# Kernel tuning notes

Hardware: AMD Instinct MI355X
Metric: run time of the kernel (lower is better)

## Reference

```python
import jax, jax.numpy as jnp
import numpy as np


def setup_inputs() -> dict:
    key = jax.random.key(0)
    ks = jax.random.split(key, 6)
    B, L, D, H, U = 256, 225, 1280, 256, 256
    features = jax.random.normal(ks[0], (B, L, D), dtype=jnp.float32)
    hidden = jax.random.normal(ks[1], (B, H), dtype=jnp.float32)
    W1 = jax.random.normal(ks[2], (D, U), dtype=jnp.float32) * (1.0 / np.sqrt(D))
    b1 = jnp.zeros((U,), dtype=jnp.float32)
    W2 = jax.random.normal(ks[3], (H, U), dtype=jnp.float32) * (1.0 / np.sqrt(H))
    b2 = jnp.zeros((U,), dtype=jnp.float32)
    V = jax.random.normal(ks[4], (U, 1), dtype=jnp.float32) * (1.0 / np.sqrt(U))
    bV = jnp.zeros((1,), dtype=jnp.float32)
    return {"features": features, "hidden": hidden, "W1": W1, "b1": b1,
            "W2": W2, "b2": b2, "V": V, "bV": bV}


def reference(features, hidden, W1, b1, W2, b2, V, bV):
    # features: [B, L, D]; hidden: [B, H]
    proj_f = jnp.einsum('bld,du->blu', features, W1) + b1        # [B, L, U]
    proj_h = (hidden @ W2 + b2)[:, None, :]                      # [B, 1, U]
    score = jnp.tanh(proj_f + proj_h)                            # [B, L, U]
    logits = jnp.einsum('blu,uo->blo', score, V) + bV            # [B, L, 1]
    attn = jax.nn.softmax(logits, axis=1)                        # [B, L, 1]
    context = jnp.sum(attn * features, axis=1)                   # [B, D]
    return context
```

## Files before the change

kernel.cpp:

```cpp
#include <hip/hip_runtime.h>
#include <hip/hip_bf16.h>

#define B_ 256
#define L_ 225
#define D_ 1280
#define H_ 256
#define U_ 256

typedef __bf16  bf16x8 __attribute__((ext_vector_type(8)));
typedef float   f32x4  __attribute__((ext_vector_type(4)));
typedef unsigned short u16x8 __attribute__((ext_vector_type(8)));

__device__ __forceinline__ unsigned short f2bf(float f) {
    union { __hip_bfloat16 h; unsigned short u; } cv;
    cv.h = __float2bfloat16(f);
    return cv.u;
}

__device__ __forceinline__ void gload_lds16(const void* g, void* l) {
    __builtin_amdgcn_global_load_lds(
        (const __attribute__((address_space(1))) unsigned int*)g,
        (__attribute__((address_space(3))) unsigned int*)l,
        16, 0, 0);
}

__device__ __forceinline__ float wredmax(float x) {
#pragma unroll
    for (int off = 32; off > 0; off >>= 1) x = fmaxf(x, __shfl_xor(x, off, 64));
    return x;
}
__device__ __forceinline__ float wredsum(float x) {
#pragma unroll
    for (int off = 32; off > 0; off >>= 1) x += __shfl_xor(x, off, 64);
    return x;
}

__global__ void k_prep_w1t(const float* __restrict__ W1, __hip_bfloat16* __restrict__ w1t) {
    int idx = blockIdx.x * 256 + threadIdx.x;
    int k = idx / U_;
    int u = idx % U_;
    w1t[(size_t)u * D_ + k] = __float2bfloat16(W1[idx]);
}

__global__ void k_proj_h(const float* __restrict__ hidden, const float* __restrict__ W2,
                         const float* __restrict__ b1, const float* __restrict__ b2,
                         float* __restrict__ ph) {
    __shared__ float sh[H_];
    int b = blockIdx.x;
    int u = threadIdx.x;
    sh[u] = hidden[b * H_ + u];
    __syncthreads();
    float acc = b1[u] + b2[u];
#pragma unroll 8
    for (int h = 0; h < H_; ++h) acc += sh[h] * W2[h * U_ + u];
    ph[b * U_ + u] = acc;
}

__global__ __launch_bounds__(1024, 4) void k_fused(
        const float* __restrict__ feat,
        const __hip_bfloat16* __restrict__ w1t,
        const float* __restrict__ ph,
        const float* __restrict__ Vv,
        float* __restrict__ out) {
    __shared__ __align__(128) char smem[139392];
    float* sV   = (float*)(smem + 131072);
    float* sPh  = (float*)(smem + 132096);
    float* sL   = (float*)(smem + 133120);
    float* sLog = (float*)(smem + 137216);
    float* sAtt = (float*)(smem + 138240);
    float* sRed = (float*)(smem + 139264);
    float* sRed2= (float*)(smem + 139328);

    const int tid  = threadIdx.x;
    const int lane = tid & 63;
    const int wave = tid >> 6;
    const int wr   = wave >> 2;
    const int wc   = wave & 3;
    const int b    = blockIdx.x;

    if (tid < 256) { sV[tid] = Vv[tid]; sPh[tid] = ph[b * 256 + tid]; }

    const int ar    = tid >> 2;
    const int arc   = ar < L_ ? ar : (L_ - 1);
    const int akseg = (tid & 3) << 4;
    const float* aSrc0 = feat + ((size_t)(b * L_ + arc) * D_ + akseg);
    const int ac80  = akseg >> 3;
    char* const aDst0 = smem;

    f32x4 acc[4][4];
#pragma unroll
    for (int mi = 0; mi < 4; ++mi)
#pragma unroll
        for (int ni = 0; ni < 4; ++ni)
            acc[mi][ni] = (f32x4){0.f, 0.f, 0.f, 0.f};

    auto stage = [&](int kt, char* bufA, char* bufB) {
        const float* src = aSrc0 + kt * 64;
        f32x4 v0 = *reinterpret_cast<const f32x4*>(src);
        f32x4 v1 = *reinterpret_cast<const f32x4*>(src + 4);
        f32x4 v2 = *reinterpret_cast<const f32x4*>(src + 8);
        f32x4 v3 = *reinterpret_cast<const f32x4*>(src + 12);
#pragma unroll
        for (int pass = 0; pass < 2; ++pass) {
            int s   = pass * 1024 + tid;
            int u   = s >> 3;
            int c8s = s & 7;
            int c8g = c8s ^ (u & 7);
            gload_lds16(w1t + (size_t)u * D_ + kt * 64 + c8g * 8, bufB + s * 16);
        }
        u16x8 w0, w1;
        w0[0] = f2bf(v0[0]); w0[1] = f2bf(v0[1]); w0[2] = f2bf(v0[2]); w0[3] = f2bf(v0[3]);
        w0[4] = f2bf(v1[0]); w0[5] = f2bf(v1[1]); w0[6] = f2bf(v1[2]); w0[7] = f2bf(v1[3]);
        w1[0] = f2bf(v2[0]); w1[1] = f2bf(v2[1]); w1[2] = f2bf(v2[2]); w1[3] = f2bf(v2[3]);
        w1[4] = f2bf(v3[0]); w1[5] = f2bf(v3[1]); w1[6] = f2bf(v3[2]); w1[7] = f2bf(v3[3]);
        int swz = (ar & 7) << 4;
        *reinterpret_cast<u16x8*>(bufA + (ar << 7) + ((ac80 << 4) ^ swz))       = w0;
        *reinterpret_cast<u16x8*>(bufA + (ar << 7) + (((ac80 + 1) << 4) ^ swz)) = w1;
    };

    auto compute = [&](const char* bufA, const char* bufB) {
#pragma unroll
        for (int ks = 0; ks < 2; ++ks) {
            const int kk2 = (ks * 32 + ((lane >> 4) << 3)) * 2;
            bf16x8 a[4], bb[4];
#pragma unroll
            for (int mi = 0; mi < 4; ++mi) {
                int r = wr * 64 + mi * 16 + (lane & 15);
                a[mi] = *reinterpret_cast<const bf16x8*>(bufA + (r << 7) + (kk2 ^ ((r & 7) << 4)));
            }
#pragma unroll
            for (int ni = 0; ni < 4; ++ni) {
                int u = wc * 64 + ni * 16 + (lane & 15);
                bb[ni] = *reinterpret_cast<const bf16x8*>(bufB + (u << 7) + (kk2 ^ ((u & 7) << 4)));
            }
#pragma unroll
            for (int mi = 0; mi < 4; ++mi)
#pragma unroll
                for (int ni = 0; ni < 4; ++ni)
                    acc[mi][ni] = __builtin_amdgcn_mfma_f32_16x16x32_bf16(
                        a[mi], bb[ni], acc[mi][ni], 0, 0, 0);
        }
    };

    stage(0, smem, smem + 32768);
    __syncthreads();
    int cur = 0;
    for (int kt = 0; kt < 20; ++kt) {
        char* An = smem + (cur ^ 1) * 65536;
        if (kt < 19) stage(kt + 1, An, An + 32768);
        char* Ac = smem + cur * 65536;
        compute(Ac, Ac + 32768);
        __syncthreads();
        cur ^= 1;
    }

    float phu[4], vu[4];
#pragma unroll
    for (int ni = 0; ni < 4; ++ni) {
        int u = wc * 64 + ni * 16 + (lane & 15);
        phu[ni] = sPh[u];
        vu[ni]  = sV[u];
    }
#pragma unroll
    for (int mi = 0; mi < 4; ++mi) {
#pragma unroll
        for (int rg = 0; rg < 4; ++rg) {
            int row = wr * 64 + mi * 16 + ((lane >> 4) << 2) + rg;
            float s = 0.f;
#pragma unroll
            for (int ni = 0; ni < 4; ++ni) {
                float x = acc[mi][ni][rg] + phu[ni];
                float t = 1.f - 2.f / (__expf(2.f * x) + 1.f);
                s += t * vu[ni];
            }
            s += __shfl_xor(s, 1, 64);
            s += __shfl_xor(s, 2, 64);
            s += __shfl_xor(s, 4, 64);
            s += __shfl_xor(s, 8, 64);
            if ((lane & 15) == 0) sL[wc * 256 + row] = s;
        }
    }
    __syncthreads();
    if (tid < 256) sLog[tid] = sL[tid] + sL[256 + tid] + sL[512 + tid] + sL[768 + tid];
    __syncthreads();

    float x  = (tid < L_) ? sLog[tid] : -3.4e38f;
    float mx = wredmax(x);
    if (lane == 0) sRed[wave] = mx;
    __syncthreads();
    mx = sRed[0];
#pragma unroll
    for (int i = 1; i < 16; ++i) mx = fmaxf(mx, sRed[i]);
    float e  = (tid < L_) ? __expf(x - mx) : 0.f;
    float sm = wredsum(e);
    if (lane == 0) sRed2[wave] = sm;
    __syncthreads();
    sm = 0.f;
#pragma unroll
    for (int i = 0; i < 16; ++i) sm += sRed2[i];
    if (tid < L_) sAtt[tid] = e / sm;
    __syncthreads();

    f32x4 c[5];
#pragma unroll
    for (int ch = 0; ch < 5; ++ch) c[ch] = (f32x4){0.f, 0.f, 0.f, 0.f};
    for (int l = wave; l < L_; l += 16) {
        float a = sAtt[l];
        const float* fr = feat + (size_t)(b * L_ + l) * D_ + (lane << 2);
#pragma unroll
        for (int ch = 0; ch < 5; ++ch)
            c[ch] += a * *reinterpret_cast<const f32x4*>(fr + ch * 256);
    }
    float* pc = (float*)smem;
#pragma unroll
    for (int ch = 0; ch < 5; ++ch)
        *reinterpret_cast<f32x4*>(pc + wave * 1280 + ch * 256 + (lane << 2)) = c[ch];
    __syncthreads();
    if (tid < 320) {
        f32x4 s = (f32x4){0.f, 0.f, 0.f, 0.f};
#pragma unroll
        for (int w = 0; w < 16; ++w)
            s += *reinterpret_cast<const f32x4*>(pc + w * 1280 + (tid << 2));
        *reinterpret_cast<f32x4*>(out + (size_t)b * D_ + (tid << 2)) = s;
    }
}

extern "C" void kernel_launch(void* const* d_in, const int* in_sizes, int n_in,
                              void* d_out, int out_size, void* d_ws, size_t ws_size,
                              hipStream_t stream) {
    const float* feat   = (const float*)d_in[0];
    const float* hidden = (const float*)d_in[1];
    const float* W1     = (const float*)d_in[2];
    const float* b1     = (const float*)d_in[3];
    const float* W2     = (const float*)d_in[4];
    const float* b2     = (const float*)d_in[5];
    const float* Vv     = (const float*)d_in[6];

    char* ws = (char*)d_ws;
    __hip_bfloat16* w1t = (__hip_bfloat16*)(ws);
    float* ph = (float*)(ws + 655360);
    float* out = (float*)d_out;

    k_prep_w1t<<<(U_ * D_) / 256, 256, 0, stream>>>(W1, w1t);
    k_proj_h  <<<B_, U_, 0, stream>>>(hidden, W2, b1, b2, ph);
    k_fused   <<<B_, 1024, 0, stream>>>(feat, w1t, ph, Vv, out);
}
```

Before: 139.1 us.

## Tile sequence into 32-row chunks with online softmax, reusing LDS features

The sequence is processed in 32-row tiles. Each tile's full-K features are converted to bf16 and held in LDS, the W1 slices are streamed through double buffers, and an online-softmax running max and sum update the context accumulators from the same LDS copy. This removes the second global pass over the large feature tensor. In exchange, W1 is re-streamed once per tile, each tile hits many block-wide barriers, and the context is accumulated from bf16 rather than fp32 features, which may matter for accuracy. The leftover row 224 goes through a separate scalar path.

```diff
diff --git a/kernel.cpp b/kernel.cpp
--- a/kernel.cpp
+++ b/kernel.cpp
@@ -6,15 +6,25 @@
 #define D_ 1280
 #define H_ 256
 #define U_ 256
+#define LT 32
+#define NFT 7
 
 typedef __bf16  bf16x8 __attribute__((ext_vector_type(8)));
 typedef float   f32x4  __attribute__((ext_vector_type(4)));
 typedef unsigned short u16x8 __attribute__((ext_vector_type(8)));
+typedef unsigned short u16x4 __attribute__((ext_vector_type(4)));
 
 __device__ __forceinline__ unsigned short f2bf(float f) {
     union { __hip_bfloat16 h; unsigned short u; } cv;
     cv.h = __float2bfloat16(f);
     return cv.u;
+}
+
+__device__ __forceinline__ f32x4 bf4_to_f32(u16x4 w) {
+    union { unsigned u; float f; } a0, a1, a2, a3;
+    a0.u = (unsigned)w[0] << 16; a1.u = (unsigned)w[1] << 16;
+    a2.u = (unsigned)w[2] << 16; a3.u = (unsigned)w[3] << 16;
+    return (f32x4){a0.f, a1.f, a2.f, a3.f};
 }
 
 __device__ __forceinline__ void gload_lds16(const void* g, void* l) {
@@ -56,161 +66,195 @@
     ph[b * U_ + u] = acc;
 }
 
+__device__ __forceinline__ void stageB(const __hip_bfloat16* __restrict__ w1t,
+                                       char* buf, int kt, int tid) {
+#pragma unroll
+    for (int pass = 0; pass < 2; ++pass) {
+        int s   = pass * 1024 + tid;
+        int u   = s >> 3;
+        int c8s = s & 7;
+        int c8g = c8s ^ (u & 7);
+        gload_lds16(w1t + (size_t)u * D_ + kt * 64 + c8g * 8, buf + s * 16);
+    }
+}
+
 __global__ __launch_bounds__(1024, 4) void k_fused(
         const float* __restrict__ feat,
         const __hip_bfloat16* __restrict__ w1t,
         const float* __restrict__ ph,
         const float* __restrict__ Vv,
         float* __restrict__ out) {
-    __shared__ __align__(128) char smem[139392];
-    float* sV   = (float*)(smem + 131072);
-    float* sPh  = (float*)(smem + 132096);
-    float* sL   = (float*)(smem + 133120);
-    float* sLog = (float*)(smem + 137216);
-    float* sAtt = (float*)(smem + 138240);
-    float* sRed = (float*)(smem + 139264);
-    float* sRed2= (float*)(smem + 139328);
+    __shared__ __align__(128) char smem[150784];
+    char*  sB  = smem + 81920;
+    float* sV  = (float*)(smem + 147456);
+    float* sPh = (float*)(smem + 148480);
+    float* sLp = (float*)(smem + 149504);
+    float* sW  = (float*)(smem + 150528);
+    float* sSc = (float*)(smem + 150656);
 
     const int tid  = threadIdx.x;
     const int lane = tid & 63;
     const int wave = tid >> 6;
-    const int wr   = wave >> 2;
-    const int wc   = wave & 3;
+    const int wr   = wave >> 3;
+    const int wc   = wave & 7;
     const int b    = blockIdx.x;
 
     if (tid < 256) { sV[tid] = Vv[tid]; sPh[tid] = ph[b * 256 + tid]; }
 
-    const int ar    = tid >> 2;
-    const int arc   = ar < L_ ? ar : (L_ - 1);
-    const int akseg = (tid & 3) << 4;
-    const float* aSrc0 = feat + ((size_t)(b * L_ + arc) * D_ + akseg);
-    const int ac80  = akseg >> 3;
-    char* const aDst0 = smem;
-
-    f32x4 acc[4][4];
-#pragma unroll
-    for (int mi = 0; mi < 4; ++mi)
-#pragma unroll
-        for (int ni = 0; ni < 4; ++ni)
-            acc[mi][ni] = (f32x4){0.f, 0.f, 0.f, 0.f};
-
-    auto stage = [&](int kt, char* bufA, char* bufB) {
-        const float* src = aSrc0 + kt * 64;
-        f32x4 v0 = *reinterpret_cast<const f32x4*>(src);
-        f32x4 v1 = *reinterpret_cast<const f32x4*>(src + 4);
-        f32x4 v2 = *reinterpret_cast<const f32x4*>(src + 8);
-        f32x4 v3 = *reinterpret_cast<const f32x4*>(src + 12);
-#pragma unroll
-        for (int pass = 0; pass < 2; ++pass) {
-            int s   = pass * 1024 + tid;
-            int u   = s >> 3;
-            int c8s = s & 7;
-            int c8g = c8s ^ (u & 7);
-            gload_lds16(w1t + (size_t)u * D_ + kt * 64 + c8g * 8, bufB + s * 16);
-        }
-        u16x8 w0, w1;
-        w0[0] = f2bf(v0[0]); w0[1] = f2bf(v0[1]); w0[2] = f2bf(v0[2]); w0[3] = f2bf(v0[3]);
-        w0[4] = f2bf(v1[0]); w0[5] = f2bf(v1[1]); w0[6] = f2bf(v1[2]); w0[7] = f2bf(v1[3]);
-        w1[0] = f2bf(v2[0]); w1[1] = f2bf(v2[1]); w1[2] = f2bf(v2[2]); w1[3] = f2bf(v2[3]);
-        w1[4] = f2bf(v3[0]); w1[5] = f2bf(v3[1]); w1[6] = f2bf(v3[2]); w1[7] = f2bf(v3[3]);
-        int swz = (ar & 7) << 4;
-        *reinterpret_cast<u16x8*>(bufA + (ar << 7) + ((ac80 << 4) ^ swz))       = w0;
-        *reinterpret_cast<u16x8*>(bufA + (ar << 7) + (((ac80 + 1) << 4) ^ swz)) = w1;
-    };
-
-    auto compute = [&](const char* bufA, const char* bufB) {
-#pragma unroll
-        for (int ks = 0; ks < 2; ++ks) {
-            const int kk2 = (ks * 32 + ((lane >> 4) << 3)) * 2;
-            bf16x8 a[4], bb[4];
-#pragma unroll
-            for (int mi = 0; mi < 4; ++mi) {
-                int r = wr * 64 + mi * 16 + (lane & 15);
-                a[mi] = *reinterpret_cast<const bf16x8*>(bufA + (r << 7) + (kk2 ^ ((r & 7) << 4)));
+    const float* featB = feat + (size_t)b * L_ * D_;
+
+    f32x4 c[5];
+#pragma unroll
+    for (int ch = 0; ch < 5; ++ch) c[ch] = (f32x4){0.f, 0.f, 0.f, 0.f};
+    float m_run = -3.0e38f, s_run = 0.f;
+
+    for (int t = 0; t < NFT; ++t) {
+        __syncthreads();
+
+#pragma unroll
+        for (int p = 0; p < 10; ++p) {
+            int idx = tid + p * 1024;
+            int r   = idx / 320;
+            int c4  = idx - r * 320;
+            f32x4 v = *reinterpret_cast<const f32x4*>(
+                featB + (size_t)(t * LT + r) * D_ + c4 * 4);
+            u16x4 w;
+            w[0] = f2bf(v[0]); w[1] = f2bf(v[1]); w[2] = f2bf(v[2]); w[3] = f2bf(v[3]);
+            *reinterpret_cast<u16x4*>(smem + r * 2560 + ((c4 * 8) ^ ((r & 7) << 4))) = w;
+        }
+        stageB(w1t, sB, 0, tid);
+        __syncthreads();
+
+        f32x4 acc0 = (f32x4){0.f, 0.f, 0.f, 0.f};
+        f32x4 acc1 = (f32x4){0.f, 0.f, 0.f, 0.f};
+        int cur = 0;
+        const int r  = wr * 16 + (lane & 15);
+        const int u0 = wc * 32 + (lane & 15);
+        const int aswz = (r & 7) << 4;
+        const int bswz = (u0 & 7) << 4;
+        for (int kt = 0; kt < 20; ++kt) {
+            if (kt < 19) stageB(w1t, sB + (cur ^ 1) * 32768, kt + 1, tid);
+            const char* bufB = sB + cur * 32768;
+#pragma unroll
+            for (int ks = 0; ks < 2; ++ks) {
+                int kloc = ks * 64 + ((lane >> 4) << 4);
+                bf16x8 a = *reinterpret_cast<const bf16x8*>(
+                    smem + r * 2560 + ((kt * 128 + kloc) ^ aswz));
+                bf16x8 b0 = *reinterpret_cast<const bf16x8*>(
+                    bufB + u0 * 128 + (kloc ^ bswz));
+                bf16x8 b1 = *reinterpret_cast<const bf16x8*>(
+                    bufB + (u0 + 16) * 128 + (kloc ^ bswz));
+                acc0 = __builtin_amdgcn_mfma_f32_16x16x32_bf16(a, b0, acc0, 0, 0, 0);
+                acc1 = __builtin_amdgcn_mfma_f32_16x16x32_bf16(a, b1, acc1, 0, 0, 0);
             }
-#pragma unroll
-            for (int ni = 0; ni < 4; ++ni) {
-                int u = wc * 64 + ni * 16 + (lane & 15);
-                bb[ni] = *reinterpret_cast<const bf16x8*>(bufB + (u << 7) + (kk2 ^ ((u & 7) << 4)));
+            __syncthreads();
+            cur ^= 1;
+        }
+
+        float ph0 = sPh[u0], ph1 = sPh[u0 + 16];
+        float v0  = sV[u0],  v1  = sV[u0 + 16];
+#pragma unroll
+        for (int rg = 0; rg < 4; ++rg) {
+            int row = wr * 16 + ((lane >> 4) << 2) + rg;
+            float x0 = acc0[rg] + ph0;
+            float x1 = acc1[rg] + ph1;
+            float sl = (1.f - 2.f / (__expf(2.f * x0) + 1.f)) * v0
+                     + (1.f - 2.f / (__expf(2.f * x1) + 1.f)) * v1;
+            sl += __shfl_xor(sl, 1, 64);
+            sl += __shfl_xor(sl, 2, 64);
+            sl += __shfl_xor(sl, 4, 64);
+            sl += __shfl_xor(sl, 8, 64);
+            if ((lane & 15) == 0) sLp[wc * 32 + row] = sl;
+        }
+        __syncthreads();
+
+        if (wave == 0) {
+            float lg = -3.0e38f;
+            if (lane < 32) {
+                lg = 0.f;
+#pragma unroll
+                for (int w8 = 0; w8 < 8; ++w8) lg += sLp[w8 * 32 + lane];
             }
-#pragma unroll
-            for (int mi = 0; mi < 4; ++mi)
-#pragma unroll
-                for (int ni = 0; ni < 4; ++ni)
-                    acc[mi][ni] = __builtin_amdgcn_mfma_f32_16x16x32_bf16(
-                        a[mi], bb[ni], acc[mi][ni], 0, 0, 0);
-        }
-    };
-
-    stage(0, smem, smem + 32768);
-    __syncthreads();
-    int cur = 0;
-    for (int kt = 0; kt < 20; ++kt) {
-        char* An = smem + (cur ^ 1) * 65536;
-        if (kt < 19) stage(kt + 1, An, An + 32768);
-        char* Ac = smem + cur * 65536;
-        compute(Ac, Ac + 32768);
-        __syncthreads();
-        cur ^= 1;
-    }
-
-    float phu[4], vu[4];
-#pragma unroll
-    for (int ni = 0; ni < 4; ++ni) {
-        int u = wc * 64 + ni * 16 + (lane & 15);
-        phu[ni] = sPh[u];
-        vu[ni]  = sV[u];
-    }
-#pragma unroll
-    for (int mi = 0; mi < 4; ++mi) {
-#pragma unroll
-        for (int rg = 0; rg < 4; ++rg) {
-            int row = wr * 64 + mi * 16 + ((lane >> 4) << 2) + rg;
-            float s = 0.f;
-#pragma unroll
-            for (int ni = 0; ni < 4; ++ni) {
-                float x = acc[mi][ni][rg] + phu[ni];
-                float t = 1.f - 2.f / (__expf(2.f * x) + 1.f);
-                s += t * vu[ni];
+            float tmax = wredmax(lg);
+            float nm   = fmaxf(m_run, tmax);
+            float wv   = (lane < 32) ? __expf(lg - nm) : 0.f;
+            float ts   = wredsum(wv);
+            float rs   = __expf(m_run - nm);
+            s_run = s_run * rs + ts;
+            m_run = nm;
+            if (lane < 32) sW[lane] = wv;
+            if (lane == 0) sSc[0] = rs;
+        }
+        __syncthreads();
+
+        float rs = sSc[0];
+#pragma unroll
+        for (int ch = 0; ch < 5; ++ch) c[ch] *= rs;
+#pragma unroll
+        for (int rp = 0; rp < 2; ++rp) {
+            int rr = wave + rp * 16;
+            float wgt = sW[rr];
+            const char* arow = smem + rr * 2560;
+            int rswz = (rr & 7) << 4;
+#pragma unroll
+            for (int ch = 0; ch < 5; ++ch) {
+                u16x4 w4 = *reinterpret_cast<const u16x4*>(
+                    arow + ((ch * 512 + lane * 8) ^ rswz));
+                c[ch] += wgt * bf4_to_f32(w4);
             }
-            s += __shfl_xor(s, 1, 64);
-            s += __shfl_xor(s, 2, 64);
-            s += __shfl_xor(s, 4, 64);
-            s += __shfl_xor(s, 8, 64);
-            if ((lane & 15) == 0) sL[wc * 256 + row] = s;
-        }
-    }
-    __syncthreads();
-    if (tid < 256) sLog[tid] = sL[tid] + sL[256 + tid] + sL[512 + tid] + sL[768 + tid];
-    __syncthreads();
-
-    float x  = (tid < L_) ? sLog[tid] : -3.4e38f;
-    float mx = wredmax(x);
-    if (lane == 0) sRed[wave] = mx;
-    __syncthreads();
-    mx = sRed[0];
-#pragma unroll
-    for (int i = 1; i < 16; ++i) mx = fmaxf(mx, sRed[i]);
-    float e  = (tid < L_) ? __expf(x - mx) : 0.f;
-    float sm = wredsum(e);
-    if (lane == 0) sRed2[wave] = sm;
-    __syncthreads();
-    sm = 0.f;
-#pragma unroll
-    for (int i = 0; i < 16; ++i) sm += sRed2[i];
-    if (tid < L_) sAtt[tid] = e / sm;
-    __syncthreads();
-
-    f32x4 c[5];
-#pragma unroll
-    for (int ch = 0; ch < 5; ++ch) c[ch] = (f32x4){0.f, 0.f, 0.f, 0.f};
-    for (int l = wave; l < L_; l += 16) {
-        float a = sAtt[l];
-        const float* fr = feat + (size_t)(b * L_ + l) * D_ + (lane << 2);
-#pragma unroll
-        for (int ch = 0; ch < 5; ++ch)
-            c[ch] += a * *reinterpret_cast<const f32x4*>(fr + ch * 256);
-    }
+        }
+    }
+
+    {
+        const float* frow = featB + (size_t)224 * D_;
+        int u  = wave * 16 + (lane & 15);
+        int kq = lane >> 4;
+        const float* fk = frow + kq * 320;
+        const __hip_bfloat16* wk = w1t + (size_t)u * D_ + kq * 320;
+        float dot = 0.f;
+#pragma unroll 8
+        for (int i = 0; i < 80; ++i) {
+            f32x4 fv = *reinterpret_cast<const f32x4*>(fk + i * 4);
+            u16x4 w4 = *reinterpret_cast<const u16x4*>(wk + i * 4);
+            f32x4 wf = bf4_to_f32(w4);
+            dot += fv[0] * wf[0] + fv[1] * wf[1] + fv[2] * wf[2] + fv[3] * wf[3];
+        }
+        dot += __shfl_xor(dot, 16, 64);
+        dot += __shfl_xor(dot, 32, 64);
+        float xg = dot + sPh[u];
+        float sv = (1.f - 2.f / (__expf(2.f * xg) + 1.f)) * sV[u];
+        sv += __shfl_xor(sv, 1, 64);
+        sv += __shfl_xor(sv, 2, 64);
+        sv += __shfl_xor(sv, 4, 64);
+        sv += __shfl_xor(sv, 8, 64);
+        if (lane == 0) sLp[wave] = sv;
+    }
+    __syncthreads();
+    if (wave == 0) {
+        float lg = 0.f;
+#pragma unroll
+        for (int i = 0; i < 16; ++i) lg += sLp[i];
+        float nm = fmaxf(m_run, lg);
+        float wv = __expf(lg - nm);
+        float rs = __expf(m_run - nm);
+        s_run = s_run * rs + wv;
+        if (lane == 0) { sSc[0] = rs; sSc[1] = s_run; sW[0] = wv; }
+    }
+    __syncthreads();
+    {
+        float rs = sSc[0];
+#pragma unroll
+        for (int ch = 0; ch < 5; ++ch) c[ch] *= rs;
+        if (wave == 0) {
+            float wgt = sW[0];
+            const float* frow = featB + (size_t)224 * D_;
+#pragma unroll
+            for (int ch = 0; ch < 5; ++ch)
+                c[ch] += wgt * *reinterpret_cast<const f32x4*>(frow + ch * 256 + lane * 4);
+        }
+    }
+
+    __syncthreads();
     float* pc = (float*)smem;
 #pragma unroll
     for (int ch = 0; ch < 5; ++ch)
@@ -221,6 +265,8 @@
 #pragma unroll
         for (int w = 0; w < 16; ++w)
             s += *reinterpret_cast<const f32x4*>(pc + w * 1280 + (tid << 2));
+        float inv = 1.f / sSc[1];
+        s *= inv;
         *reinterpret_cast<f32x4*>(out + (size_t)b * D_ + (tid << 2)) = s;
     }
 }
```

Result: slower. 336.8 us (+142.2%).

## Spill bf16 features to workspace for context pass; drop softmax max-subtraction

Applied to the files above, without the earlier changes.

During the GEMM staging, each block writes its bf16-converted feature tile to a workspace buffer. The context-sum pass then rereads that half-size bf16 copy instead of the fp32 features, which roughly halves the second read, at the cost of an extra global write of the same size. The softmax skips the max reduction and normalizes once at the end, which removes several barriers but risks overflow for large logits. The A-tile LDS store is moved after the MFMA compute to overlap global loads, and the context loop is unrolled by two rows.

```diff
diff --git a/kernel.cpp b/kernel.cpp
--- a/kernel.cpp
+++ b/kernel.cpp
@@ -10,11 +10,19 @@
 typedef __bf16  bf16x8 __attribute__((ext_vector_type(8)));
 typedef float   f32x4  __attribute__((ext_vector_type(4)));
 typedef unsigned short u16x8 __attribute__((ext_vector_type(8)));
+typedef unsigned short u16x4 __attribute__((ext_vector_type(4)));
 
 __device__ __forceinline__ unsigned short f2bf(float f) {
     union { __hip_bfloat16 h; unsigned short u; } cv;
     cv.h = __float2bfloat16(f);
     return cv.u;
+}
+
+__device__ __forceinline__ f32x4 bf4_to_f32(u16x4 w) {
+    union { unsigned u; float f; } a0, a1, a2, a3;
+    a0.u = (unsigned)w[0] << 16; a1.u = (unsigned)w[1] << 16;
+    a2.u = (unsigned)w[2] << 16; a3.u = (unsigned)w[3] << 16;
+    return (f32x4){a0.f, a1.f, a2.f, a3.f};
 }
 
 __device__ __forceinline__ void gload_lds16(const void* g, void* l) {
@@ -24,11 +32,6 @@
         16, 0, 0);
 }
 
-__device__ __forceinline__ float wredmax(float x) {
-#pragma unroll
-    for (int off = 32; off > 0; off >>= 1) x = fmaxf(x, __shfl_xor(x, off, 64));
-    return x;
-}
 __device__ __forceinline__ float wredsum(float x) {
 #pragma unroll
     for (int off = 32; off > 0; off >>= 1) x += __shfl_xor(x, off, 64);
@@ -56,20 +59,22 @@
     ph[b * U_ + u] = acc;
 }
 
-__global__ __launch_bounds__(1024, 4) void k_fused(
+__global__ __launch_bounds__(1024) void __attribute__((noinline)) k_dummy() {}
+
+template<int BF16WS>
+__global__ __launch_bounds__(1024) void k_fused(
         const float* __restrict__ feat,
         const __hip_bfloat16* __restrict__ w1t,
         const float* __restrict__ ph,
         const float* __restrict__ Vv,
+        __hip_bfloat16* __restrict__ fbf,
         float* __restrict__ out) {
-    __shared__ __align__(128) char smem[139392];
+    __shared__ __align__(128) char smem[138304];
     float* sV   = (float*)(smem + 131072);
     float* sPh  = (float*)(smem + 132096);
     float* sL   = (float*)(smem + 133120);
-    float* sLog = (float*)(smem + 137216);
-    float* sAtt = (float*)(smem + 138240);
-    float* sRed = (float*)(smem + 139264);
-    float* sRed2= (float*)(smem + 139328);
+    float* sW   = (float*)(smem + 137216);
+    float* sRed = (float*)(smem + 138240);
 
     const int tid  = threadIdx.x;
     const int lane = tid & 63;
@@ -84,8 +89,9 @@
     const int arc   = ar < L_ ? ar : (L_ - 1);
     const int akseg = (tid & 3) << 4;
     const float* aSrc0 = feat + ((size_t)(b * L_ + arc) * D_ + akseg);
-    const int ac80  = akseg >> 3;
-    char* const aDst0 = smem;
+    __hip_bfloat16* fDst0 = fbf + ((size_t)(b * L_ + arc) * D_ + akseg);
+    const int ac80 = akseg >> 3;
+    const int aswz = (ar & 7) << 4;
 
     f32x4 acc[4][4];
 #pragma unroll
@@ -94,12 +100,14 @@
         for (int ni = 0; ni < 4; ++ni)
             acc[mi][ni] = (f32x4){0.f, 0.f, 0.f, 0.f};
 
-    auto stage = [&](int kt, char* bufA, char* bufB) {
+    auto loadA = [&](int kt, f32x4* v) {
         const float* src = aSrc0 + kt * 64;
-        f32x4 v0 = *reinterpret_cast<const f32x4*>(src);
-        f32x4 v1 = *reinterpret_cast<const f32x4*>(src + 4);
-        f32x4 v2 = *reinterpret_cast<const f32x4*>(src + 8);
-        f32x4 v3 = *reinterpret_cast<const f32x4*>(src + 12);
+        v[0] = *reinterpret_cast<const f32x4*>(src);
+        v[1] = *reinterpret_cast<const f32x4*>(src + 4);
+        v[2] = *reinterpret_cast<const f32x4*>(src + 8);
+        v[3] = *reinterpret_cast<const f32x4*>(src + 12);
+    };
+    auto stageB = [&](int kt, char* bufB) {
 #pragma unroll
         for (int pass = 0; pass < 2; ++pass) {
             int s   = pass * 1024 + tid;
@@ -108,16 +116,20 @@
             int c8g = c8s ^ (u & 7);
             gload_lds16(w1t + (size_t)u * D_ + kt * 64 + c8g * 8, bufB + s * 16);
         }
+    };
+    auto storeA = [&](int kt, const f32x4* v, char* bufA) {
         u16x8 w0, w1;
-        w0[0] = f2bf(v0[0]); w0[1] = f2bf(v0[1]); w0[2] = f2bf(v0[2]); w0[3] = f2bf(v0[3]);
-        w0[4] = f2bf(v1[0]); w0[5] = f2bf(v1[1]); w0[6] = f2bf(v1[2]); w0[7] = f2bf(v1[3]);
-        w1[0] = f2bf(v2[0]); w1[1] = f2bf(v2[1]); w1[2] = f2bf(v2[2]); w1[3] = f2bf(v2[3]);
-        w1[4] = f2bf(v3[0]); w1[5] = f2bf(v3[1]); w1[6] = f2bf(v3[2]); w1[7] = f2bf(v3[3]);
-        int swz = (ar & 7) << 4;
-        *reinterpret_cast<u16x8*>(bufA + (ar << 7) + ((ac80 << 4) ^ swz))       = w0;
-        *reinterpret_cast<u16x8*>(bufA + (ar << 7) + (((ac80 + 1) << 4) ^ swz)) = w1;
+        w0[0] = f2bf(v[0][0]); w0[1] = f2bf(v[0][1]); w0[2] = f2bf(v[0][2]); w0[3] = f2bf(v[0][3]);
+        w0[4] = f2bf(v[1][0]); w0[5] = f2bf(v[1][1]); w0[6] = f2bf(v[1][2]); w0[7] = f2bf(v[1][3]);
+        w1[0] = f2bf(v[2][0]); w1[1] = f2bf(v[2][1]); w1[2] = f2bf(v[2][2]); w1[3] = f2bf(v[2][3]);
+        w1[4] = f2bf(v[3][0]); w1[5] = f2bf(v[3][1]); w1[6] = f2bf(v[3][2]); w1[7] = f2bf(v[3][3]);
+        *reinterpret_cast<u16x8*>(bufA + (ar << 7) + ((ac80 << 4) ^ aswz))       = w0;
+        *reinterpret_cast<u16x8*>(bufA + (ar << 7) + (((ac80 + 1) << 4) ^ aswz)) = w1;
+        if (BF16WS && ar < L_) {
+            *reinterpret_cast<u16x8*>(fDst0 + kt * 64)     = w0;
+            *reinterpret_cast<u16x8*>(fDst0 + kt * 64 + 8) = w1;
+        }
     };
-
     auto compute = [&](const char* bufA, const char* bufB) {
 #pragma unroll
         for (int ks = 0; ks < 2; ++ks) {
@@ -142,14 +154,21 @@
         }
     };
 
-    stage(0, smem, smem + 32768);
+    {
+        f32x4 v[4];
+        loadA(0, v);
+        stageB(0, smem + 32768);
+        storeA(0, v, smem);
+    }
     __syncthreads();
     int cur = 0;
     for (int kt = 0; kt < 20; ++kt) {
-        char* An = smem + (cur ^ 1) * 65536;
-        if (kt < 19) stage(kt + 1, An, An + 32768);
-        char* Ac = smem + cur * 65536;
-        compute(Ac, Ac + 32768);
+        char* bufN = smem + (cur ^ 1) * 65536;
+        f32x4 v[4];
+        if (kt < 19) { loadA(kt + 1, v); stageB(kt + 1, bufN + 32768); }
+        char* bufC = smem + cur * 65536;
+        compute(bufC, bufC + 32768);
+        if (kt < 19) storeA(kt + 1, v, bufN);
         __syncthreads();
         cur ^= 1;
     }
@@ -170,8 +189,7 @@
 #pragma unroll
             for (int ni = 0; ni < 4; ++ni) {
                 float x = acc[mi][ni][rg] + phu[ni];
-                float t = 1.f - 2.f / (__expf(2.f * x) + 1.f);
-                s += t * vu[ni];
+                s += (1.f - 2.f / (__expf(2.f * x) + 1.f)) * vu[ni];
             }
             s += __shfl_xor(s, 1, 64);
             s += __shfl_xor(s, 2, 64);
@@ -181,46 +199,100 @@
         }
     }
     __syncthreads();
-    if (tid < 256) sLog[tid] = sL[tid] + sL[256 + tid] + sL[512 + tid] + sL[768 + tid];
-    __syncthreads();
-
-    float x  = (tid < L_) ? sLog[tid] : -3.4e38f;
-    float mx = wredmax(x);
-    if (lane == 0) sRed[wave] = mx;
-    __syncthreads();
-    mx = sRed[0];
-#pragma unroll
-    for (int i = 1; i < 16; ++i) mx = fmaxf(mx, sRed[i]);
-    float e  = (tid < L_) ? __expf(x - mx) : 0.f;
-    float sm = wredsum(e);
-    if (lane == 0) sRed2[wave] = sm;
-    __syncthreads();
-    sm = 0.f;
-#pragma unroll
-    for (int i = 0; i < 16; ++i) sm += sRed2[i];
-    if (tid < L_) sAtt[tid] = e / sm;
+    float den_p = 0.f;
+    if (tid < 256) {
+        float lg = sL[tid] + sL[256 + tid] + sL[512 + tid] + sL[768 + tid];
+        float w  = (tid < L_) ? __expf(lg) : 0.f;
+        sW[tid] = w;
+        den_p = w;
+    }
+    den_p = wredsum(den_p);
+    if (lane == 0) sRed[wave] = den_p;
     __syncthreads();
 
     f32x4 c[5];
 #pragma unroll
     for (int ch = 0; ch < 5; ++ch) c[ch] = (f32x4){0.f, 0.f, 0.f, 0.f};
-    for (int l = wave; l < L_; l += 16) {
-        float a = sAtt[l];
-        const float* fr = feat + (size_t)(b * L_ + l) * D_ + (lane << 2);
+
+    if (BF16WS) {
+        const char* fB = (const char*)(fbf + (size_t)b * L_ * D_);
+        int l = wave;
+        for (; l + 16 < L_; l += 32) {
+            float wa = sW[l], wb = sW[l + 16];
+            const char* ra = fB + (size_t)l * 2560;
+            const char* rb = fB + (size_t)(l + 16) * 2560;
+            u16x8 a0 = *reinterpret_cast<const u16x8*>(ra + lane * 16);
+            u16x8 a1 = *reinterpret_cast<const u16x8*>(ra + 1024 + lane * 16);
+            u16x4 a2 = *reinterpret_cast<const u16x4*>(ra + 2048 + lane * 8);
+            u16x8 b0 = *reinterpret_cast<const u16x8*>(rb + lane * 16);
+            u16x8 b1 = *reinterpret_cast<const u16x8*>(rb + 1024 + lane * 16);
+            u16x4 b2 = *reinterpret_cast<const u16x4*>(rb + 2048 + lane * 8);
+            c[0] += wa * bf4_to_f32((u16x4){a0[0],a0[1],a0[2],a0[3]});
+            c[1] += wa * bf4_to_f32((u16x4){a0[4],a0[5],a0[6],a0[7]});
+            c[2] += wa * bf4_to_f32((u16x4){a1[0],a1[1],a1[2],a1[3]});
+            c[3] += wa * bf4_to_f32((u16x4){a1[4],a1[5],a1[6],a1[7]});
+            c[4] += wa * bf4_to_f32(a2);
+            c[0] += wb * bf4_to_f32((u16x4){b0[0],b0[1],b0[2],b0[3]});
+            c[1] += wb * bf4_to_f32((u16x4){b0[4],b0[5],b0[6],b0[7]});
+            c[2] += wb * bf4_to_f32((u16x4){b1[0],b1[1],b1[2],b1[3]});
+            c[3] += wb * bf4_to_f32((u16x4){b1[4],b1[5],b1[6],b1[7]});
+            c[4] += wb * bf4_to_f32(b2);
+        }
+        if (l < L_) {
+            float wa = sW[l];
+            const char* ra = fB + (size_t)l * 2560;
+            u16x8 a0 = *reinterpret_cast<const u16x8*>(ra + lane * 16);
+            u16x8 a1 = *reinterpret_cast<const u16x8*>(ra + 1024 + lane * 16);
+            u16x4 a2 = *reinterpret_cast<const u16x4*>(ra + 2048 + lane * 8);
+            c[0] += wa * bf4_to_f32((u16x4){a0[0],a0[1],a0[2],a0[3]});
+            c[1] += wa * bf4_to_f32((u16x4){a0[4],a0[5],a0[6],a0[7]});
+            c[2] += wa * bf4_to_f32((u16x4){a1[0],a1[1],a1[2],a1[3]});
+            c[3] += wa * bf4_to_f32((u16x4){a1[4],a1[5],a1[6],a1[7]});
+            c[4] += wa * bf4_to_f32(a2);
+        }
+    } else {
+        const float* fB = feat + (size_t)b * L_ * D_;
+        int l = wave;
+        for (; l + 16 < L_; l += 32) {
+            float wa = sW[l], wb = sW[l + 16];
+            const float* ra = fB + (size_t)l * D_ + (lane << 2);
+            const float* rb = fB + (size_t)(l + 16) * D_ + (lane << 2);
+#pragma unroll
+            for (int ch = 0; ch < 5; ++ch) {
+                c[ch] += wa * *reinterpret_cast<const f32x4*>(ra + ch * 256);
+                c[ch] += wb * *reinterpret_cast<const f32x4*>(rb + ch * 256);
+            }
+        }
+        if (l < L_) {
+            float wa = sW[l];
+            const float* ra = fB + (size_t)l * D_ + (lane << 2);
+#pragma unroll
+            for (int ch = 0; ch < 5; ++ch)
+                c[ch] += wa * *reinterpret_cast<const f32x4*>(ra + ch * 256);
+        }
+    }
+
+    float* pc = (float*)smem;
+    if (BF16WS) {
+#pragma unroll
+        for (int ch = 0; ch < 4; ++ch)
+            *reinterpret_cast<f32x4*>(pc + wave * 1280 + (ch >> 1) * 512 + lane * 8 + (ch & 1) * 4) = c[ch];
+        *reinterpret_cast<f32x4*>(pc + wave * 1280 + 1024 + lane * 4) = c[4];
+    } else {
 #pragma unroll
         for (int ch = 0; ch < 5; ++ch)
-            c[ch] += a * *reinterpret_cast<const f32x4*>(fr + ch * 256);
-    }
-    float* pc = (float*)smem;
-#pragma unroll
-    for (int ch = 0; ch < 5; ++ch)
-        *reinterpret_cast<f32x4*>(pc + wave * 1280 + ch * 256 + (lane << 2)) = c[ch];
+            *reinterpret_cast<f32x4*>(pc + wave * 1280 + ch * 256 + (lane << 2)) = c[ch];
+    }
     __syncthreads();
     if (tid < 320) {
         f32x4 s = (f32x4){0.f, 0.f, 0.f, 0.f};
 #pragma unroll
         for (int w = 0; w < 16; ++w)
             s += *reinterpret_cast<const f32x4*>(pc + w * 1280 + (tid << 2));
+        float den = 0.f;
+#pragma unroll
+        for (int i = 0; i < 16; ++i) den += sRed[i];
+        s *= (1.f / den);
         *reinterpret_cast<f32x4*>(out + (size_t)b * D_ + (tid << 2)) = s;
     }
 }
@@ -238,10 +310,16 @@
 
     char* ws = (char*)d_ws;
     __hip_bfloat16* w1t = (__hip_bfloat16*)(ws);
-    float* ph = (float*)(ws + 655360);
+    float* ph           = (float*)(ws + 655360);
+    __hip_bfloat16* fbf = (__hip_bfloat16*)(ws + 917504);
     float* out = (float*)d_out;
+
+    const size_t need = 917504ull + (size_t)B_ * L_ * D_ * 2ull;
 
     k_prep_w1t<<<(U_ * D_) / 256, 256, 0, stream>>>(W1, w1t);
     k_proj_h  <<<B_, U_, 0, stream>>>(hidden, W2, b1, b2, ph);
-    k_fused   <<<B_, 1024, 0, stream>>>(feat, w1t, ph, Vv, out);
-}
+    if (ws_size >= need)
+        k_fused<1><<<B_, 1024, 0, stream>>>(feat, w1t, ph, Vv, fbf, out);
+    else
+        k_fused<0><<<B_, 1024, 0, stream>>>(feat, w1t, ph, Vv, fbf, out);
+}
```

After: 146.7 us. 1.06x slower.

## Split sequence across blocks and reuse LDS-cached bf16 features for context

Applied to the files above, without the earlier changes.

Each batch row is now split into five 45-row sequence chunks, one block per chunk, for 1280 blocks. Each block loads its whole feature slice into LDS as bf16 once. That slice feeds both the W1 projection MFMAs and the attention-weighted context sum, so features are no longer read a second time from global memory. The softmax becomes unnormalized exp weights per chunk, with partial numerators and denominators merged by a new combine kernel; it skips the max subtraction and sums the context from bf16-rounded features. The whole tile is loaded up front with no overlap against compute, and the large LDS footprint limits occupancy.

```diff
diff --git a/kernel.cpp b/kernel.cpp
--- a/kernel.cpp
+++ b/kernel.cpp
@@ -6,10 +6,13 @@
 #define D_ 1280
 #define H_ 256
 #define U_ 256
+#define LT 45
+#define LTP 48
 
 typedef __bf16  bf16x8 __attribute__((ext_vector_type(8)));
 typedef float   f32x4  __attribute__((ext_vector_type(4)));
 typedef unsigned short u16x8 __attribute__((ext_vector_type(8)));
+typedef unsigned short u16x4 __attribute__((ext_vector_type(4)));
 
 __device__ __forceinline__ unsigned short f2bf(float f) {
     union { __hip_bfloat16 h; unsigned short u; } cv;
@@ -17,18 +20,13 @@
     return cv.u;
 }
 
-__device__ __forceinline__ void gload_lds16(const void* g, void* l) {
-    __builtin_amdgcn_global_load_lds(
-        (const __attribute__((address_space(1))) unsigned int*)g,
-        (__attribute__((address_space(3))) unsigned int*)l,
-        16, 0, 0);
-}
-
-__device__ __forceinline__ float wredmax(float x) {
-#pragma unroll
-    for (int off = 32; off > 0; off >>= 1) x = fmaxf(x, __shfl_xor(x, off, 64));
-    return x;
-}
+__device__ __forceinline__ f32x4 bf4_to_f32(u16x4 w) {
+    union { unsigned u; float f; } a0, a1, a2, a3;
+    a0.u = (unsigned)w[0] << 16; a1.u = (unsigned)w[1] << 16;
+    a2.u = (unsigned)w[2] << 16; a3.u = (unsigned)w[3] << 16;
+    return (f32x4){a0.f, a1.f, a2.f, a3.f};
+}
+
 __device__ __forceinline__ float wredsum(float x) {
 #pragma unroll
     for (int off = 32; off > 0; off >>= 1) x += __shfl_xor(x, off, 64);
@@ -56,161 +54,157 @@
     ph[b * U_ + u] = acc;
 }
 
-__global__ __launch_bounds__(1024, 4) void k_fused(
+__global__ __launch_bounds__(512) void k_fused(
         const float* __restrict__ feat,
         const __hip_bfloat16* __restrict__ w1t,
         const float* __restrict__ ph,
         const float* __restrict__ Vv,
-        float* __restrict__ out) {
-    __shared__ __align__(128) char smem[139392];
-    float* sV   = (float*)(smem + 131072);
-    float* sPh  = (float*)(smem + 132096);
-    float* sL   = (float*)(smem + 133120);
-    float* sLog = (float*)(smem + 137216);
-    float* sAtt = (float*)(smem + 138240);
-    float* sRed = (float*)(smem + 139264);
-    float* sRed2= (float*)(smem + 139328);
+        float* __restrict__ num,
+        float* __restrict__ den) {
+    __shared__ __align__(128) char smem[159424];
+    char*  sB  = smem + 122880;
+    float* sV  = (float*)(smem + 155648);
+    float* sPh = (float*)(smem + 156672);
+    float* sL  = (float*)(smem + 157696);
+    float* sW  = (float*)(smem + 159232);
 
     const int tid  = threadIdx.x;
     const int lane = tid & 63;
     const int wave = tid >> 6;
-    const int wr   = wave >> 2;
-    const int wc   = wave & 3;
-    const int b    = blockIdx.x;
+    const int blk  = blockIdx.x;
+    const int b    = blk / 5;
+    const int s5   = blk - b * 5;
+    const int l0   = s5 * LT;
 
     if (tid < 256) { sV[tid] = Vv[tid]; sPh[tid] = ph[b * 256 + tid]; }
 
-    const int ar    = tid >> 2;
-    const int arc   = ar < L_ ? ar : (L_ - 1);
-    const int akseg = (tid & 3) << 4;
-    const float* aSrc0 = feat + ((size_t)(b * L_ + arc) * D_ + akseg);
-    const int ac80  = akseg >> 3;
-    char* const aDst0 = smem;
-
-    f32x4 acc[4][4];
-#pragma unroll
-    for (int mi = 0; mi < 4; ++mi)
-#pragma unroll
-        for (int ni = 0; ni < 4; ++ni)
-            acc[mi][ni] = (f32x4){0.f, 0.f, 0.f, 0.f};
-
-    auto stage = [&](int kt, char* bufA, char* bufB) {
-        const float* src = aSrc0 + kt * 64;
+    const float* featB = feat + ((size_t)b * L_ + l0) * D_;
+
+#pragma unroll
+    for (int p = 0; p < 15; ++p) {
+        int id  = p * 512 + tid;
+        int row = id / 160;
+        int c8  = id - row * 160;
+        int rc  = row < LT ? row : (LT - 1);
+        const float* src = featB + (size_t)rc * D_ + c8 * 8;
         f32x4 v0 = *reinterpret_cast<const f32x4*>(src);
         f32x4 v1 = *reinterpret_cast<const f32x4*>(src + 4);
-        f32x4 v2 = *reinterpret_cast<const f32x4*>(src + 8);
-        f32x4 v3 = *reinterpret_cast<const f32x4*>(src + 12);
-#pragma unroll
-        for (int pass = 0; pass < 2; ++pass) {
-            int s   = pass * 1024 + tid;
-            int u   = s >> 3;
-            int c8s = s & 7;
-            int c8g = c8s ^ (u & 7);
-            gload_lds16(w1t + (size_t)u * D_ + kt * 64 + c8g * 8, bufB + s * 16);
-        }
-        u16x8 w0, w1;
-        w0[0] = f2bf(v0[0]); w0[1] = f2bf(v0[1]); w0[2] = f2bf(v0[2]); w0[3] = f2bf(v0[3]);
-        w0[4] = f2bf(v1[0]); w0[5] = f2bf(v1[1]); w0[6] = f2bf(v1[2]); w0[7] = f2bf(v1[3]);
-        w1[0] = f2bf(v2[0]); w1[1] = f2bf(v2[1]); w1[2] = f2bf(v2[2]); w1[3] = f2bf(v2[3]);
-        w1[4] = f2bf(v3[0]); w1[5] = f2bf(v3[1]); w1[6] = f2bf(v3[2]); w1[7] = f2bf(v3[3]);
-        int swz = (ar & 7) << 4;
-        *reinterpret_cast<u16x8*>(bufA + (ar << 7) + ((ac80 << 4) ^ swz))       = w0;
-        *reinterpret_cast<u16x8*>(bufA + (ar << 7) + (((ac80 + 1) << 4) ^ swz)) = w1;
-    };
-
-    auto compute = [&](const char* bufA, const char* bufB) {
+        u16x8 w;
+        w[0] = f2bf(v0[0]); w[1] = f2bf(v0[1]); w[2] = f2bf(v0[2]); w[3] = f2bf(v0[3]);
+        w[4] = f2bf(v1[0]); w[5] = f2bf(v1[1]); w[6] = f2bf(v1[2]); w[7] = f2bf(v1[3]);
+        *reinterpret_cast<u16x8*>(smem + row * 2560 + ((c8 * 16) ^ ((row & 7) << 4))) = w;
+    }
+
+    const __hip_bfloat16* bSrc[4];
+    int bDst[4];
+#pragma unroll
+    for (int pass = 0; pass < 4; ++pass) {
+        int sI  = pass * 512 + tid;
+        int u   = sI >> 3;
+        int c8s = sI & 7;
+        int c8g = c8s ^ (u & 7);
+        bSrc[pass] = w1t + (size_t)u * D_ + c8g * 8;
+        bDst[pass] = sI * 16;
+    }
+    u16x8 breg[4];
+#pragma unroll
+    for (int pass = 0; pass < 4; ++pass)
+        breg[pass] = *reinterpret_cast<const u16x8*>(bSrc[pass]);
+
+    f32x4 acc[3][2];
+#pragma unroll
+    for (int mi = 0; mi < 3; ++mi)
+#pragma unroll
+        for (int ni = 0; ni < 2; ++ni)
+            acc[mi][ni] = (f32x4){0.f, 0.f, 0.f, 0.f};
+
+    const int u0   = wave * 32 + (lane & 15);
+    const int bswz0 = (u0 & 7) << 4;
+    const int bswz1 = ((u0 + 16) & 7) << 4;
+    __syncthreads();
+
+    for (int kt = 0; kt < 20; ++kt) {
+#pragma unroll
+        for (int pass = 0; pass < 4; ++pass)
+            *reinterpret_cast<u16x8*>(sB + bDst[pass]) = breg[pass];
+        if (kt < 19) {
+#pragma unroll
+            for (int pass = 0; pass < 4; ++pass)
+                breg[pass] = *reinterpret_cast<const u16x8*>(bSrc[pass] + (kt + 1) * 64);
+        }
+        __syncthreads();
 #pragma unroll
         for (int ks = 0; ks < 2; ++ks) {
-            const int kk2 = (ks * 32 + ((lane >> 4) << 3)) * 2;
-            bf16x8 a[4], bb[4];
-#pragma unroll
-            for (int mi = 0; mi < 4; ++mi) {
-                int r = wr * 64 + mi * 16 + (lane & 15);
-                a[mi] = *reinterpret_cast<const bf16x8*>(bufA + (r << 7) + (kk2 ^ ((r & 7) << 4)));
+            const int kloc = ks * 64 + ((lane >> 4) << 4);
+            bf16x8 a[3], bb[2];
+#pragma unroll
+            for (int mi = 0; mi < 3; ++mi) {
+                int r = mi * 16 + (lane & 15);
+                a[mi] = *reinterpret_cast<const bf16x8*>(
+                    smem + r * 2560 + ((kt * 128 + kloc) ^ ((r & 7) << 4)));
             }
-#pragma unroll
-            for (int ni = 0; ni < 4; ++ni) {
-                int u = wc * 64 + ni * 16 + (lane & 15);
-                bb[ni] = *reinterpret_cast<const bf16x8*>(bufB + (u << 7) + (kk2 ^ ((u & 7) << 4)));
-            }
-#pragma unroll
-            for (int mi = 0; mi < 4; ++mi)
-#pragma unroll
-                for (int ni = 0; ni < 4; ++ni)
+            bb[0] = *reinterpret_cast<const bf16x8*>(sB + u0 * 128 + (kloc ^ bswz0));
+            bb[1] = *reinterpret_cast<const bf16x8*>(sB + (u0 + 16) * 128 + (kloc ^ bswz1));
+#pragma unroll
+            for (int mi = 0; mi < 3; ++mi)
+#pragma unroll
+                for (int ni = 0; ni < 2; ++ni)
                     acc[mi][ni] = __builtin_amdgcn_mfma_f32_16x16x32_bf16(
                         a[mi], bb[ni], acc[mi][ni], 0, 0, 0);
         }
-    };
-
-    stage(0, smem, smem + 32768);
-    __syncthreads();
-    int cur = 0;
-    for (int kt = 0; kt < 20; ++kt) {
-        char* An = smem + (cur ^ 1) * 65536;
-        if (kt < 19) stage(kt + 1, An, An + 32768);
-        char* Ac = smem + cur * 65536;
-        compute(Ac, Ac + 32768);
         __syncthreads();
-        cur ^= 1;
-    }
-
-    float phu[4], vu[4];
-#pragma unroll
-    for (int ni = 0; ni < 4; ++ni) {
-        int u = wc * 64 + ni * 16 + (lane & 15);
-        phu[ni] = sPh[u];
-        vu[ni]  = sV[u];
-    }
-#pragma unroll
-    for (int mi = 0; mi < 4; ++mi) {
+    }
+
+    float ph0 = sPh[u0], ph1 = sPh[u0 + 16];
+    float v0  = sV[u0],  v1  = sV[u0 + 16];
+#pragma unroll
+    for (int mi = 0; mi < 3; ++mi) {
 #pragma unroll
         for (int rg = 0; rg < 4; ++rg) {
-            int row = wr * 64 + mi * 16 + ((lane >> 4) << 2) + rg;
-            float s = 0.f;
-#pragma unroll
-            for (int ni = 0; ni < 4; ++ni) {
-                float x = acc[mi][ni][rg] + phu[ni];
-                float t = 1.f - 2.f / (__expf(2.f * x) + 1.f);
-                s += t * vu[ni];
-            }
-            s += __shfl_xor(s, 1, 64);
-            s += __shfl_xor(s, 2, 64);
-            s += __shfl_xor(s, 4, 64);
-            s += __shfl_xor(s, 8, 64);
-            if ((lane & 15) == 0) sL[wc * 256 + row] = s;
-        }
-    }
-    __syncthreads();
-    if (tid < 256) sLog[tid] = sL[tid] + sL[256 + tid] + sL[512 + tid] + sL[768 + tid];
-    __syncthreads();
-
-    float x  = (tid < L_) ? sLog[tid] : -3.4e38f;
-    float mx = wredmax(x);
-    if (lane == 0) sRed[wave] = mx;
-    __syncthreads();
-    mx = sRed[0];
-#pragma unroll
-    for (int i = 1; i < 16; ++i) mx = fmaxf(mx, sRed[i]);
-    float e  = (tid < L_) ? __expf(x - mx) : 0.f;
-    float sm = wredsum(e);
-    if (lane == 0) sRed2[wave] = sm;
-    __syncthreads();
-    sm = 0.f;
-#pragma unroll
-    for (int i = 0; i < 16; ++i) sm += sRed2[i];
-    if (tid < L_) sAtt[tid] = e / sm;
+            int row = mi * 16 + ((lane >> 4) << 2) + rg;
+            float x0 = acc[mi][0][rg] + ph0;
+            float x1 = acc[mi][1][rg] + ph1;
+            float sl = (1.f - 2.f / (__expf(2.f * x0) + 1.f)) * v0
+                     + (1.f - 2.f / (__expf(2.f * x1) + 1.f)) * v1;
+            sl += __shfl_xor(sl, 1, 64);
+            sl += __shfl_xor(sl, 2, 64);
+            sl += __shfl_xor(sl, 4, 64);
+            sl += __shfl_xor(sl, 8, 64);
+            if ((lane & 15) == 0) sL[wave * LTP + row] = sl;
+        }
+    }
+    __syncthreads();
+
+    if (wave == 0) {
+        float w = 0.f;
+        if (lane < LT) {
+            float lg = 0.f;
+#pragma unroll
+            for (int wc = 0; wc < 8; ++wc) lg += sL[wc * LTP + lane];
+            w = __expf(lg);
+            sW[lane] = w;
+        }
+        float d = wredsum(w);
+        if (lane == 0) den[blk] = d;
+    }
     __syncthreads();
 
     f32x4 c[5];
 #pragma unroll
     for (int ch = 0; ch < 5; ++ch) c[ch] = (f32x4){0.f, 0.f, 0.f, 0.f};
-    for (int l = wave; l < L_; l += 16) {
-        float a = sAtt[l];
-        const float* fr = feat + (size_t)(b * L_ + l) * D_ + (lane << 2);
-#pragma unroll
-        for (int ch = 0; ch < 5; ++ch)
-            c[ch] += a * *reinterpret_cast<const f32x4*>(fr + ch * 256);
-    }
+    for (int l = wave; l < LT; l += 8) {
+        float wgt = sW[l];
+        const char* arow = smem + l * 2560;
+        int rswz = (l & 7) << 4;
+#pragma unroll
+        for (int ch = 0; ch < 5; ++ch) {
+            u16x4 w4 = *reinterpret_cast<const u16x4*>(
+                arow + ((ch * 512 + lane * 8) ^ rswz));
+            c[ch] += wgt * bf4_to_f32(w4);
+        }
+    }
+    __syncthreads();
+
     float* pc = (float*)smem;
 #pragma unroll
     for (int ch = 0; ch < 5; ++ch)
@@ -219,10 +213,25 @@
     if (tid < 320) {
         f32x4 s = (f32x4){0.f, 0.f, 0.f, 0.f};
 #pragma unroll
-        for (int w = 0; w < 16; ++w)
+        for (int w = 0; w < 8; ++w)
             s += *reinterpret_cast<const f32x4*>(pc + w * 1280 + (tid << 2));
-        *reinterpret_cast<f32x4*>(out + (size_t)b * D_ + (tid << 2)) = s;
-    }
+        *reinterpret_cast<f32x4*>(num + (size_t)blk * 1280 + (tid << 2)) = s;
+    }
+}
+
+__global__ void k_combine(const float* __restrict__ num, const float* __restrict__ den,
+                          float* __restrict__ out) {
+    int b = blockIdx.x;
+    int t = threadIdx.x;
+    f32x4 n = (f32x4){0.f, 0.f, 0.f, 0.f};
+    float d = 0.f;
+#pragma unroll
+    for (int s = 0; s < 5; ++s) {
+        n += *reinterpret_cast<const f32x4*>(num + (size_t)(b * 5 + s) * 1280 + (t << 2));
+        d += den[b * 5 + s];
+    }
+    n *= (1.f / d);
+    *reinterpret_cast<f32x4*>(out + (size_t)b * D_ + (t << 2)) = n;
 }
 
 extern "C" void kernel_launch(void* const* d_in, const int* in_sizes, int n_in,
@@ -238,10 +247,13 @@
 
     char* ws = (char*)d_ws;
     __hip_bfloat16* w1t = (__hip_bfloat16*)(ws);
-    float* ph = (float*)(ws + 655360);
+    float* ph  = (float*)(ws + 655360);
+    float* num = (float*)(ws + 917504);
+    float* den = (float*)(ws + 7471104);
     float* out = (float*)d_out;
 
     k_prep_w1t<<<(U_ * D_) / 256, 256, 0, stream>>>(W1, w1t);
     k_proj_h  <<<B_, U_, 0, stream>>>(hidden, W2, b1, b2, ph);
-    k_fused   <<<B_, 1024, 0, stream>>>(feat, w1t, ph, Vv, out);
-}
+    k_fused   <<<B_ * 5, 512, 0, stream>>>(feat, w1t, ph, Vv, num, den);
+    k_combine <<<B_, 320, 0, stream>>>(num, den, out);
+}
```

Result: slower. 147.0 us (+5.7%).
